# Performance work log

Hardware: AMD Instinct MI355X
Metric: run time of the kernel (lower is better)

Reference implementation:

```python
import jax, jax.numpy as jnp
import numpy as np

B, C = 32, 2048

def setup_inputs() -> dict:
    key = jax.random.key(0)
    k1, k2, k3 = jax.random.split(key, 3)
    x1 = jax.random.normal(k1, (B, C), dtype=jnp.float32)
    x2 = jax.random.normal(k2, (B, C), dtype=jnp.float32)
    # 1x1 conv over 2C->C channels on a 1x1 spatial map == dense layer (C, 2C)
    W = jax.random.normal(k3, (C, 2 * C), dtype=jnp.float32) * (1.0 / np.sqrt(2 * C))
    b = jnp.zeros((C,), dtype=jnp.float32)
    return {"x1": x1, "x2": x2, "W": W, "b": b}


def reference(x1, x2, W, b):
    # conv1x1 fusion of the two (B,C) inputs -> (B,C)
    x = jnp.concatenate([x1, x2], axis=1) @ W.T + b  # (B, C)
    # energy[b,i,j] = x[b,i] * x[b,j]  (H*W == 1 -> rank-1 outer product)
    energy = x[:, :, None] * x[:, None, :]  # (B, C, C)
    # max-subtraction variant: softmax(max_j(energy) - energy) along last dim
    energy_new = jnp.max(energy, axis=-1, keepdims=True) - energy
    attention = jax.nn.softmax(energy_new, axis=-1)  # (B, C, C)
    # attention @ value (value is (B,C,1) since H=W=1) -> matvec, then residual
    out1 = jnp.einsum('bij,bj->bi', attention, x1) + x1  # (B, C)
    out2 = jnp.einsum('bij,bj->bi', attention, x2) + x2  # (B, C)
    return out1, out2, attention
```

## Files before the change

kernel.cpp:

```cpp
#include <hip/hip_runtime.h>

#define CDIM 2048
#define BATCH 32
#define K2 4096

typedef float f32x4 __attribute__((ext_vector_type(4)));

#define BN 64
#define BK 128
#define KT (K2 / BK)
#define NT (CDIM / BN)

__global__ __launch_bounds__(256) void gemm_partial_k(
    const float* __restrict__ x1, const float* __restrict__ x2,
    const float* __restrict__ W, float* __restrict__ partial)
{
    __shared__ float lds[BN * BK + BATCH * BK];
    float* Wt = lds;
    float* Xs = lds + BN * BK;

    const int nt = blockIdx.x, kt = blockIdx.y;
    const int i0 = nt * BN, k0 = kt * BK;
    const int t = threadIdx.x;
    const int lane = t & 63, ks = t >> 6;
    const int cg = lane & 7, bg = lane >> 3;

    const float* xsrc = (k0 < CDIM) ? x1 : x2;
    const int kk0 = k0 & (CDIM - 1);

    #pragma unroll
    for (int r = 0; r < 8; ++r) {
        int f = t + 256 * r;
        int row = f >> 5, kc = f & 31;
        float4 v = *reinterpret_cast<const float4*>(W + (size_t)(i0 + row) * K2 + k0 + kc * 4);
        int sc = kc ^ ((row >> 3) & 7);
        *reinterpret_cast<float4*>(&Wt[row * BK + sc * 4]) = v;
    }
    #pragma unroll
    for (int r = 0; r < 4; ++r) {
        int f = t + 256 * r;
        int row = f >> 5, kc = f & 31;
        float4 v = *reinterpret_cast<const float4*>(xsrc + row * CDIM + kk0 + kc * 4);
        int sc = kc ^ ((row >> 2) & 7);
        *reinterpret_cast<float4*>(&Xs[row * BK + sc * 4]) = v;
    }
    __syncthreads();

    float acc[4][8] = {};
    #pragma unroll 2
    for (int s = 0; s < 8; ++s) {
        const int kc = ks * 8 + s;
        f32x4 xv[4], wv[8];
        #pragma unroll
        for (int bb = 0; bb < 4; ++bb)
            xv[bb] = *reinterpret_cast<const f32x4*>(&Xs[(4 * bg + bb) * BK + (kc ^ bg) * 4]);
        #pragma unroll
        for (int cc = 0; cc < 8; ++cc)
            wv[cc] = *reinterpret_cast<const f32x4*>(&Wt[(8 * cg + cc) * BK + (kc ^ cg) * 4]);
        #pragma unroll
        for (int bb = 0; bb < 4; ++bb)
            #pragma unroll
            for (int cc = 0; cc < 8; ++cc)
                #pragma unroll
                for (int w = 0; w < 4; ++w)
                    acc[bb][cc] = fmaf(xv[bb][w], wv[cc][w], acc[bb][cc]);
    }

    __syncthreads();
    float* accS = lds;
    #pragma unroll
    for (int bb = 0; bb < 4; ++bb)
        #pragma unroll
        for (int cc = 0; cc < 8; ++cc)
            accS[(ks * 64 + lane) * 33 + bb * 8 + cc] = acc[bb][cc];
    __syncthreads();

    {
        const int l0 = t >> 2, q = t & 3;
        float s0[8];
        #pragma unroll
        for (int j = 0; j < 8; ++j) {
            float s = 0.f;
            #pragma unroll
            for (int k = 0; k < 4; ++k)
                s += accS[(k * 64 + l0) * 33 + q * 8 + j];
            s0[j] = s;
        }
        const int b_row = 4 * (l0 >> 3) + q;
        const int icol  = 8 * (l0 & 7);
        float* dst = partial + (size_t)kt * (BATCH * CDIM) + b_row * CDIM + i0 + icol;
        float4 lo = make_float4(s0[0], s0[1], s0[2], s0[3]);
        float4 hi = make_float4(s0[4], s0[5], s0[6], s0[7]);
        *reinterpret_cast<float4*>(dst)     = lo;
        *reinterpret_cast<float4*>(dst + 4) = hi;
    }
}

__global__ __launch_bounds__(256) void reduce_x_k(
    const float* __restrict__ partial, const float* __restrict__ bias,
    float* __restrict__ x)
{
    int idx = blockIdx.x * 256 + threadIdx.x;
    float s = 0.f;
    #pragma unroll
    for (int kt = 0; kt < KT; ++kt) s += partial[(size_t)kt * (BATCH * CDIM) + idx];
    x[idx] = s + bias[idx & (CDIM - 1)];
}

__global__ __launch_bounds__(256) void attn_k(
    const float* __restrict__ x, const float* __restrict__ x1,
    const float* __restrict__ x2, float* __restrict__ out1,
    float* __restrict__ out2, float* __restrict__ att)
{
    __shared__ float xs[CDIM];
    __shared__ float xs1[CDIM];
    __shared__ float xs2[CDIM];
    __shared__ float wred[8];
    const int b = blockIdx.x >> 5, rg = blockIdx.x & 31;
    const int t = threadIdx.x;
    const int lane = t & 63, wv = t >> 6;
    const float* xb  = x  + b * CDIM;
    const float* x1b = x1 + b * CDIM;
    const float* x2b = x2 + b * CDIM;

    #pragma unroll
    for (int r = 0; r < 2; ++r) {
        int f = (t + 256 * r) * 4;
        *reinterpret_cast<float4*>(&xs[f])  = *reinterpret_cast<const float4*>(xb  + f);
        *reinterpret_cast<float4*>(&xs1[f]) = *reinterpret_cast<const float4*>(x1b + f);
        *reinterpret_cast<float4*>(&xs2[f]) = *reinterpret_cast<const float4*>(x2b + f);
    }
    __syncthreads();

    float mn = 1e30f, mx = -1e30f;
    for (int f = t; f < CDIM; f += 256) {
        float v = xs[f];
        mn = fminf(mn, v); mx = fmaxf(mx, v);
    }
    #pragma unroll
    for (int off = 32; off > 0; off >>= 1) {
        mn = fminf(mn, __shfl_xor(mn, off));
        mx = fmaxf(mx, __shfl_xor(mx, off));
    }
    if (lane == 0) { wred[wv] = mn; wred[4 + wv] = mx; }
    __syncthreads();
    mn = fminf(fminf(wred[0], wred[1]), fminf(wred[2], wred[3]));
    mx = fmaxf(fmaxf(wred[4], wred[5]), fmaxf(wred[6], wred[7]));

    for (int r = 0; r < 16; ++r) {
        const int i = rg * 64 + wv * 16 + r;
        const float xi = xs[i];
        const float li = (xi >= 0.f) ? xi * mn : xi * mx;
        const float nxi = -xi;
        float sum = 0.f, d1 = 0.f, d2 = 0.f;
        #pragma unroll
        for (int g = 0; g < 8; ++g) {
            const int o = g * 256 + lane * 4;
            f32x4 xv = *reinterpret_cast<const f32x4*>(&xs[o]);
            f32x4 v1 = *reinterpret_cast<const f32x4*>(&xs1[o]);
            f32x4 v2 = *reinterpret_cast<const f32x4*>(&xs2[o]);
            #pragma unroll
            for (int c = 0; c < 4; ++c) {
                float ev = __expf(fmaf(nxi, xv[c], li));
                sum += ev;
                d1 = fmaf(ev, v1[c], d1);
                d2 = fmaf(ev, v2[c], d2);
            }
        }
        #pragma unroll
        for (int off = 32; off > 0; off >>= 1) {
            sum += __shfl_xor(sum, off);
            d1  += __shfl_xor(d1, off);
            d2  += __shfl_xor(d2, off);
        }
        const float inv = 1.f / sum;
        if (lane == 0) {
            out1[b * CDIM + i] = fmaf(d1, inv, xs1[i]);
            out2[b * CDIM + i] = fmaf(d2, inv, xs2[i]);
        }
        float* arow = att + (size_t)(b * CDIM + i) * CDIM;
        #pragma unroll
        for (int g = 0; g < 8; ++g) {
            const int o = g * 256 + lane * 4;
            f32x4 xv = *reinterpret_cast<const f32x4*>(&xs[o]);
            f32x4 v;
            #pragma unroll
            for (int c = 0; c < 4; ++c)
                v[c] = __expf(fmaf(nxi, xv[c], li)) * inv;
            *reinterpret_cast<f32x4*>(arow + o) = v;
        }
    }
}

extern "C" void kernel_launch(void* const* d_in, const int* in_sizes, int n_in,
                              void* d_out, int out_size, void* d_ws, size_t ws_size,
                              hipStream_t stream) {
    const float* x1   = (const float*)d_in[0];
    const float* x2   = (const float*)d_in[1];
    const float* W    = (const float*)d_in[2];
    const float* bias = (const float*)d_in[3];
    float* out  = (float*)d_out;
    float* out1 = out;
    float* out2 = out + BATCH * CDIM;
    float* att  = out + 2 * BATCH * CDIM;
    float* x    = (float*)d_ws;

    float* partial = out + ((size_t)out_size - (size_t)KT * BATCH * CDIM);

    gemm_partial_k<<<dim3(NT, KT), dim3(256), 0, stream>>>(x1, x2, W, partial);
    reduce_x_k<<<(BATCH * CDIM) / 256, 256, 0, stream>>>(partial, bias, x);
    attn_k<<<BATCH * (CDIM / 64), 256, 0, stream>>>(x, x1, x2, out1, out2, att);
}
```

Baseline: 123.0 us.

## Fuse GEMM, reduction and attention into one cooperative persistent kernel

Replaces the three separate launches (split-K GEMM, partial reduction, attention) with a single cooperative kernel of 512 blocks that uses grid-wide syncs between phases. Each block processes two GEMM tiles, a slice of the reduction, and two attention row groups. The aim is to remove launch overhead and inter-kernel gaps. In exchange it pays for two grid barriers and a fixed grid size that may underuse the GPU in the attention phase. If the cooperative launch fails, it falls back to the original three kernels.

After: 244.3 us. 98.5% more time.

```diff
diff --git a/kernel.cpp b/kernel.cpp
--- a/kernel.cpp
+++ b/kernel.cpp
@@ -1,15 +1,19 @@
 #include <hip/hip_runtime.h>
+#include <hip/hip_cooperative_groups.h>
+
+namespace cg = cooperative_groups;
 
 #define CDIM 2048
 #define BATCH 32
 #define K2 4096
-
-typedef float f32x4 __attribute__((ext_vector_type(4)));
-
 #define BN 64
 #define BK 128
 #define KT (K2 / BK)
 #define NT (CDIM / BN)
+#define GRID 512
+
+typedef float f32x4 __attribute__((ext_vector_type(4)));
+
 
 __global__ __launch_bounds__(256) void gemm_partial_k(
     const float* __restrict__ x1, const float* __restrict__ x2,
@@ -23,7 +27,7 @@
     const int i0 = nt * BN, k0 = kt * BK;
     const int t = threadIdx.x;
     const int lane = t & 63, ks = t >> 6;
-    const int cg = lane & 7, bg = lane >> 3;
+    const int cg8 = lane & 7, bg = lane >> 3;
 
     const float* xsrc = (k0 < CDIM) ? x1 : x2;
     const int kk0 = k0 & (CDIM - 1);
@@ -56,7 +60,7 @@
             xv[bb] = *reinterpret_cast<const f32x4*>(&Xs[(4 * bg + bb) * BK + (kc ^ bg) * 4]);
         #pragma unroll
         for (int cc = 0; cc < 8; ++cc)
-            wv[cc] = *reinterpret_cast<const f32x4*>(&Wt[(8 * cg + cc) * BK + (kc ^ cg) * 4]);
+            wv[cc] = *reinterpret_cast<const f32x4*>(&Wt[(8 * cg8 + cc) * BK + (kc ^ cg8) * 4]);
         #pragma unroll
         for (int bb = 0; bb < 4; ++bb)
             #pragma unroll
@@ -89,10 +93,8 @@
         const int b_row = 4 * (l0 >> 3) + q;
         const int icol  = 8 * (l0 & 7);
         float* dst = partial + (size_t)kt * (BATCH * CDIM) + b_row * CDIM + i0 + icol;
-        float4 lo = make_float4(s0[0], s0[1], s0[2], s0[3]);
-        float4 hi = make_float4(s0[4], s0[5], s0[6], s0[7]);
-        *reinterpret_cast<float4*>(dst)     = lo;
-        *reinterpret_cast<float4*>(dst + 4) = hi;
+        *reinterpret_cast<float4*>(dst)     = make_float4(s0[0], s0[1], s0[2], s0[3]);
+        *reinterpret_cast<float4*>(dst + 4) = make_float4(s0[4], s0[5], s0[6], s0[7]);
     }
 }
 
@@ -192,6 +194,206 @@
     }
 }
 
+__global__ __launch_bounds__(256, 2) void fused_k(
+    const float* __restrict__ x1, const float* __restrict__ x2,
+    const float* __restrict__ W, const float* __restrict__ bias,
+    float* __restrict__ out1, float* __restrict__ out2,
+    float* __restrict__ att, float* __restrict__ partial,
+    float* __restrict__ xrow)
+{
+    __shared__ float lds[BN * BK + BATCH * BK];
+    const int t = threadIdx.x;
+    const int lane = t & 63, wv = t >> 6;
+    cg::grid_group grid = cg::this_grid();
+
+    {
+        float* Wt = lds;
+        float* Xs = lds + BN * BK;
+        const int ks = wv;
+        const int cg8 = lane & 7, bg = lane >> 3;
+
+        #pragma unroll
+        for (int tile = 0; tile < 2; ++tile) {
+            const int tau = blockIdx.x + tile * GRID;
+            const int nt = tau & 31, kt = tau >> 5;
+            const int i0 = nt * BN, k0 = kt * BK;
+            const float* xsrc = (k0 < CDIM) ? x1 : x2;
+            const int kk0 = k0 & (CDIM - 1);
+
+            #pragma unroll
+            for (int r = 0; r < 8; ++r) {
+                int f = t + 256 * r;
+                int row = f >> 5, kc = f & 31;
+                float4 v = *reinterpret_cast<const float4*>(
+                    W + (size_t)(i0 + row) * K2 + k0 + kc * 4);
+                int sc = kc ^ ((row >> 3) & 7);
+                *reinterpret_cast<float4*>(&Wt[row * BK + sc * 4]) = v;
+            }
+            #pragma unroll
+            for (int r = 0; r < 4; ++r) {
+                int f = t + 256 * r;
+                int row = f >> 5, kc = f & 31;
+                float4 v = *reinterpret_cast<const float4*>(
+                    xsrc + row * CDIM + kk0 + kc * 4);
+                int sc = kc ^ ((row >> 2) & 7);
+                *reinterpret_cast<float4*>(&Xs[row * BK + sc * 4]) = v;
+            }
+            __syncthreads();
+
+            float acc[4][8] = {};
+            #pragma unroll 2
+            for (int s = 0; s < 8; ++s) {
+                const int kc = ks * 8 + s;
+                f32x4 xv[4], wvv[8];
+                #pragma unroll
+                for (int bb = 0; bb < 4; ++bb)
+                    xv[bb] = *reinterpret_cast<const f32x4*>(
+                        &Xs[(4 * bg + bb) * BK + (kc ^ bg) * 4]);
+                #pragma unroll
+                for (int cc = 0; cc < 8; ++cc)
+                    wvv[cc] = *reinterpret_cast<const f32x4*>(
+                        &Wt[(8 * cg8 + cc) * BK + (kc ^ cg8) * 4]);
+                #pragma unroll
+                for (int bb = 0; bb < 4; ++bb)
+                    #pragma unroll
+                    for (int cc = 0; cc < 8; ++cc)
+                        #pragma unroll
+                        for (int w = 0; w < 4; ++w)
+                            acc[bb][cc] = fmaf(xv[bb][w], wvv[cc][w], acc[bb][cc]);
+            }
+
+            __syncthreads();
+            float* accS = lds;
+            #pragma unroll
+            for (int bb = 0; bb < 4; ++bb)
+                #pragma unroll
+                for (int cc = 0; cc < 8; ++cc)
+                    accS[(ks * 64 + lane) * 33 + bb * 8 + cc] = acc[bb][cc];
+            __syncthreads();
+
+            {
+                const int l0 = t >> 2, q = t & 3;
+                float s0[8];
+                #pragma unroll
+                for (int j = 0; j < 8; ++j) {
+                    float s = 0.f;
+                    #pragma unroll
+                    for (int k = 0; k < 4; ++k)
+                        s += accS[(k * 64 + l0) * 33 + q * 8 + j];
+                    s0[j] = s;
+                }
+                const int b_row = 4 * (l0 >> 3) + q;
+                const int icol  = 8 * (l0 & 7);
+                float* dst = partial + (size_t)kt * (BATCH * CDIM)
+                             + b_row * CDIM + i0 + icol;
+                *reinterpret_cast<float4*>(dst) =
+                    make_float4(s0[0], s0[1], s0[2], s0[3]);
+                *reinterpret_cast<float4*>(dst + 4) =
+                    make_float4(s0[4], s0[5], s0[6], s0[7]);
+            }
+            __syncthreads();
+        }
+    }
+
+    grid.sync();
+
+    if (t < 128) {
+        const int idx = blockIdx.x * 128 + t;
+        float s = 0.f;
+        #pragma unroll
+        for (int kt = 0; kt < KT; ++kt)
+            s += partial[(size_t)kt * (BATCH * CDIM) + idx];
+        xrow[idx] = s + bias[idx & (CDIM - 1)];
+    }
+
+    grid.sync();
+
+    {
+        float* xs   = lds;
+        float* xs1  = lds + CDIM;
+        float* xs2  = lds + 2 * CDIM;
+        float* wred = lds + 3 * CDIM;
+
+        #pragma unroll
+        for (int u = 0; u < 2; ++u) {
+            const int unit = blockIdx.x * 2 + u;
+            const int b = unit >> 5, rg = unit & 31;
+            const float* xb  = xrow + b * CDIM;
+            const float* x1b = x1 + b * CDIM;
+            const float* x2b = x2 + b * CDIM;
+
+            __syncthreads();
+            #pragma unroll
+            for (int r = 0; r < 2; ++r) {
+                int f = (t + 256 * r) * 4;
+                *reinterpret_cast<float4*>(&xs[f])  = *reinterpret_cast<const float4*>(xb  + f);
+                *reinterpret_cast<float4*>(&xs1[f]) = *reinterpret_cast<const float4*>(x1b + f);
+                *reinterpret_cast<float4*>(&xs2[f]) = *reinterpret_cast<const float4*>(x2b + f);
+            }
+            __syncthreads();
+
+            float mn = 1e30f, mx = -1e30f;
+            for (int f = t; f < CDIM; f += 256) {
+                float v = xs[f];
+                mn = fminf(mn, v); mx = fmaxf(mx, v);
+            }
+            #pragma unroll
+            for (int off = 32; off > 0; off >>= 1) {
+                mn = fminf(mn, __shfl_xor(mn, off));
+                mx = fmaxf(mx, __shfl_xor(mx, off));
+            }
+            if (lane == 0) { wred[wv] = mn; wred[4 + wv] = mx; }
+            __syncthreads();
+            mn = fminf(fminf(wred[0], wred[1]), fminf(wred[2], wred[3]));
+            mx = fmaxf(fmaxf(wred[4], wred[5]), fmaxf(wred[6], wred[7]));
+
+            for (int r = 0; r < 16; ++r) {
+                const int i = rg * 64 + wv * 16 + r;
+                const float xi = xs[i];
+                const float li = (xi >= 0.f) ? xi * mn : xi * mx;
+                const float nxi = -xi;
+                float sum = 0.f, d1 = 0.f, d2 = 0.f;
+                #pragma unroll
+                for (int g = 0; g < 8; ++g) {
+                    const int o = g * 256 + lane * 4;
+                    f32x4 xv = *reinterpret_cast<const f32x4*>(&xs[o]);
+                    f32x4 v1 = *reinterpret_cast<const f32x4*>(&xs1[o]);
+                    f32x4 v2 = *reinterpret_cast<const f32x4*>(&xs2[o]);
+                    #pragma unroll
+                    for (int c = 0; c < 4; ++c) {
+                        float ev = __expf(fmaf(nxi, xv[c], li));
+                        sum += ev;
+                        d1 = fmaf(ev, v1[c], d1);
+                        d2 = fmaf(ev, v2[c], d2);
+                    }
+                }
+                #pragma unroll
+                for (int off = 32; off > 0; off >>= 1) {
+                    sum += __shfl_xor(sum, off);
+                    d1  += __shfl_xor(d1, off);
+                    d2  += __shfl_xor(d2, off);
+                }
+                const float inv = 1.f / sum;
+                if (lane == 0) {
+                    out1[b * CDIM + i] = fmaf(d1, inv, xs1[i]);
+                    out2[b * CDIM + i] = fmaf(d2, inv, xs2[i]);
+                }
+                float* arow = att + (size_t)(b * CDIM + i) * CDIM;
+                #pragma unroll
+                for (int g = 0; g < 8; ++g) {
+                    const int o = g * 256 + lane * 4;
+                    f32x4 xv = *reinterpret_cast<const f32x4*>(&xs[o]);
+                    f32x4 v;
+                    #pragma unroll
+                    for (int c = 0; c < 4; ++c)
+                        v[c] = __expf(fmaf(nxi, xv[c], li)) * inv;
+                    *reinterpret_cast<f32x4*>(arow + o) = v;
+                }
+            }
+        }
+    }
+}
+
 extern "C" void kernel_launch(void* const* d_in, const int* in_sizes, int n_in,
                               void* d_out, int out_size, void* d_ws, size_t ws_size,
                               hipStream_t stream) {
@@ -203,11 +405,20 @@
     float* out1 = out;
     float* out2 = out + BATCH * CDIM;
     float* att  = out + 2 * BATCH * CDIM;
-    float* x    = (float*)d_ws;
+    float* xrow = (float*)d_ws;
 
     float* partial = out + ((size_t)out_size - (size_t)KT * BATCH * CDIM);
 
-    gemm_partial_k<<<dim3(NT, KT), dim3(256), 0, stream>>>(x1, x2, W, partial);
-    reduce_x_k<<<(BATCH * CDIM) / 256, 256, 0, stream>>>(partial, bias, x);
-    attn_k<<<BATCH * (CDIM / 64), 256, 0, stream>>>(x, x1, x2, out1, out2, att);
+    void* args[] = {(void*)&x1, (void*)&x2, (void*)&W, (void*)&bias,
+                    (void*)&out1, (void*)&out2, (void*)&att,
+                    (void*)&partial, (void*)&xrow};
+    hipError_t err = hipLaunchCooperativeKernel((const void*)fused_k,
+                                                dim3(GRID), dim3(256),
+                                                args, 0, stream);
+    if (err != hipSuccess) {
+        (void)hipGetLastError();
+        gemm_partial_k<<<dim3(NT, KT), dim3(256), 0, stream>>>(x1, x2, W, partial);
+        reduce_x_k<<<(BATCH * CDIM) / 256, 256, 0, stream>>>(partial, bias, xrow);
+        attn_k<<<BATCH * (CDIM / 64), 256, 0, stream>>>(xrow, x1, x2, out1, out2, att);
+    }
 }
```
